# Kernel tuning notes

Measured on AMD Instinct MI355X. Metric: run time of the kernel, lower is better.

The kernel has to match this reference:

```python
import jax, jax.numpy as jnp
import numpy as np

N, T, C_IN, H, C_OUT = 50000, 8, 32, 128, 32
E = 800000


def setup_inputs() -> dict:
    key = jax.random.key(0)
    ks = jax.random.split(key, 16)
    s = 0.05
    return {
        "x": jax.random.normal(ks[0], (N, T, C_IN), dtype=jnp.float32),
        "edge_index": jax.random.randint(ks[1], (2, E), 0, N, dtype=jnp.int64),
        # SAGEConv: lin_l applied to mean-aggregated neighbors (with bias), lin_r to root (no bias)
        "Wl": jax.random.normal(ks[2], (H, C_IN), dtype=jnp.float32) * s,
        "bl": jnp.zeros((H,), dtype=jnp.float32),
        "Wr": jax.random.normal(ks[3], (H, C_IN), dtype=jnp.float32) * s,
        # GRU (torch layout: gates stacked [r; z; n])
        "W_ih": jax.random.normal(ks[4], (3 * H, H), dtype=jnp.float32) * s,
        "b_ih": jnp.zeros((3 * H,), dtype=jnp.float32),
        "W_hh": jax.random.normal(ks[5], (3 * H, H), dtype=jnp.float32) * s,
        "b_hh": jnp.zeros((3 * H,), dtype=jnp.float32),
        # heads
        "W_rec": jax.random.normal(ks[6], (C_OUT, H), dtype=jnp.float32) * s,
        "b_rec": jnp.zeros((C_OUT,), dtype=jnp.float32),
        "W_c1": jax.random.normal(ks[7], (H // 2, H), dtype=jnp.float32) * s,
        "b_c1": jnp.zeros((H // 2,), dtype=jnp.float32),
        "W_c2": jax.random.normal(ks[8], (1, H // 2), dtype=jnp.float32) * s,
        "b_c2": jnp.zeros((1,), dtype=jnp.float32),
    }


def _st_graph_sage(x, edge_index, Wl, bl, Wr, W_ih, b_ih, W_hh, b_hh,
                   W_rec, b_rec, W_c1, b_c1, W_c2, b_c2):
    n_nodes = x.shape[0]
    src, dst = edge_index[0], edge_index[1]
    # in-degree for mean aggregation (avoid div-by-zero for isolated nodes)
    deg = jax.ops.segment_sum(jnp.ones_like(dst, dtype=x.dtype), dst,
                              num_segments=n_nodes)
    deg = jnp.maximum(deg, 1.0)[:, None]
    hdim = W_hh.shape[1]

    def step(h, x_t):
        # SAGEConv (mean aggr): lin_l(mean_j x_j) + lin_r(x_i)
        agg = jax.ops.segment_sum(x_t[src], dst, num_segments=n_nodes) / deg
        sp = jax.nn.relu(agg @ Wl.T + bl + x_t @ Wr.T)
        # single-step GRU (torch equations)
        gx = sp @ W_ih.T + b_ih
        gh = h @ W_hh.T + b_hh
        gx_r, gx_z, gx_n = jnp.split(gx, 3, axis=-1)
        gh_r, gh_z, gh_n = jnp.split(gh, 3, axis=-1)
        r = jax.nn.sigmoid(gx_r + gh_r)
        z = jax.nn.sigmoid(gx_z + gh_z)
        n = jnp.tanh(gx_n + r * gh_n)
        h_new = (1.0 - z) * n + z * h
        return h_new, h_new

    h0 = jnp.zeros((n_nodes, hdim), dtype=x.dtype)
    _, hs = jax.lax.scan(step, h0, jnp.transpose(x, (1, 0, 2)))  # hs: [T, N, H]

    recon = hs @ W_rec.T + b_rec                                  # [T, N, C_OUT]
    cls = jax.nn.sigmoid(jax.nn.relu(hs @ W_c1.T + b_c1) @ W_c2.T + b_c2)  # [T, N, 1]
    reconstruction_output = jnp.transpose(recon, (1, 0, 2))       # [N, T, C_OUT]
    classification_output = jnp.transpose(cls[..., 0], (1, 0))    # [N, T]
    return reconstruction_output, classification_output


def reference(x, edge_index, Wl, bl, Wr, W_ih, b_ih, W_hh, b_hh,
              W_rec, b_rec, W_c1, b_c1, W_c2, b_c2):
    return _st_graph_sage(x, edge_index, Wl, bl, Wr, W_ih, b_ih, W_hh, b_hh,
                          W_rec, b_rec, W_c1, b_c1, W_c2, b_c2)
```

## Files before the change

kernel.cpp:

```cpp
#include <hip/hip_runtime.h>
#include <hip/hip_bf16.h>

#define N_NODES 50000
#define T_STEPS 8
#define CIN     32
#define HDIM    128
#define E_EDGES 800000
#define NBLK    196

typedef __attribute__((ext_vector_type(8))) short  short8;
typedef __attribute__((ext_vector_type(4))) float  f32x4;

__device__ __forceinline__ ushort f2b(float f) {
    __hip_bfloat16 b = __float2bfloat16(f);
    return *reinterpret_cast<ushort*>(&b);
}
__device__ __forceinline__ float b2f(ushort u) { return __uint_as_float(((uint)u) << 16); }
__device__ __forceinline__ float sigm(float x)  { return 1.f / (1.f + __expf(-x)); }
__device__ __forceinline__ float tanhx(float x) { float e = __expf(2.f * x); return 1.f - 2.f / (e + 1.f); }
__device__ __forceinline__ int SW(int fl) { return fl ^ (fl >> 3); }

__global__ void k_deg(const int* __restrict__ ei, int* __restrict__ deg) {
    int e = blockIdx.x * 256 + threadIdx.x;
    if (e < E_EDGES) atomicAdd(&deg[ei[E_EDGES + e]], 1);
}

__global__ __launch_bounds__(256)
void k_scan1(const int* __restrict__ deg, int* __restrict__ incl, int* __restrict__ bsum) {
    __shared__ int sA[256], sB[256];
    int tid = threadIdx.x;
    int i = blockIdx.x * 256 + tid;
    sA[tid] = (i < N_NODES) ? deg[i] : 0;
    __syncthreads();
    int* rd = sA; int* wr = sB;
    for (int off = 1; off < 256; off <<= 1) {
        int v = rd[tid];
        if (tid >= off) v += rd[tid - off];
        wr[tid] = v;
        __syncthreads();
        int* tmp = rd; rd = wr; wr = tmp;
    }
    incl[i] = rd[tid];
    if (tid == 255) bsum[blockIdx.x] = rd[255];
}

__global__ void k_scan2(const int* __restrict__ bsum, int* __restrict__ boff,
                        int* __restrict__ row_ptr) {
    __shared__ int sA[256], sB[256];
    int tid = threadIdx.x;
    int v0 = (tid < NBLK) ? bsum[tid] : 0;
    sA[tid] = v0;
    __syncthreads();
    int* rd = sA; int* wr = sB;
    for (int off = 1; off < 256; off <<= 1) {
        int v = rd[tid];
        if (tid >= off) v += rd[tid - off];
        wr[tid] = v;
        __syncthreads();
        int* tmp = rd; rd = wr; wr = tmp;
    }
    if (tid < NBLK) boff[tid] = rd[tid] - v0;
    if (tid == NBLK - 1) row_ptr[N_NODES] = rd[tid];
}

__global__ __launch_bounds__(256)
void k_scan3(const int* __restrict__ deg, const int* __restrict__ incl,
             const int* __restrict__ boff, int* __restrict__ row_ptr,
             int* __restrict__ cursor, float* __restrict__ rdeg) {
    int i = blockIdx.x * 256 + threadIdx.x;
    if (i >= N_NODES) return;
    int d = deg[i];
    int excl = incl[i] - d + boff[blockIdx.x];
    row_ptr[i] = excl;
    cursor[i]  = excl;
    rdeg[i] = 1.0f / (float)max(d, 1);
}

__global__ void k_bucket(const int* __restrict__ ei, int* __restrict__ cursor,
                         int* __restrict__ csr_src) {
    int e = blockIdx.x * 256 + threadIdx.x;
    if (e < E_EDGES) {
        int d = ei[E_EDGES + e];
        int slot = atomicAdd(&cursor[d], 1);
        csr_src[slot] = ei[e];
    }
}

__global__ __launch_bounds__(256)
void k_xbf(const float* __restrict__ x, ushort* __restrict__ xb) {
    size_t i = ((size_t)blockIdx.x * 256 + threadIdx.x) * 4;
    float4 v = *(const float4*)(x + i);
    ushort4 o; o.x = f2b(v.x); o.y = f2b(v.y); o.z = f2b(v.z); o.w = f2b(v.w);
    *(ushort4*)(xb + i) = o;
}

__global__ void k_pack(const float* __restrict__ Wih, const float* __restrict__ Whh,
                       const float* __restrict__ Wl,  const float* __restrict__ Wr,
                       const float* __restrict__ Wrec,const float* __restrict__ Wc1,
                       short* __restrict__ Bf, short* __restrict__ Bsf, short* __restrict__ B2f) {
    int i = blockIdx.x * 256 + threadIdx.x;
    if (i < 65536) {
        int b = i & 7, lane = (i >> 3) & 63, ks = (i >> 9) & 7, ct = i >> 12;
        int col = ct * 16 + (lane & 15);
        int k = ks * 32 + ((lane >> 4) << 3) + b;
        float v = (k < 128) ? Wih[col * 128 + k] : Whh[col * 128 + (k - 128)];
        Bf[i] = (short)f2b(v);
    } else if (i < 81920) {
        int t2 = i - 65536;
        int b = t2 & 7, lane = (t2 >> 3) & 63, ks = (t2 >> 9) & 3, ct = t2 >> 11;
        int col = 256 + ct * 16 + (lane & 15);
        int k = ks * 32 + ((lane >> 4) << 3) + b;
        Bf[i] = (short)f2b(Wih[col * 128 + k]);
    } else if (i < 98304) {
        int t2 = i - 81920;
        int b = t2 & 7, lane = (t2 >> 3) & 63, ks = (t2 >> 9) & 3, ct = t2 >> 11;
        int col = 256 + ct * 16 + (lane & 15);
        int k = ks * 32 + ((lane >> 4) << 3) + b;
        Bf[i] = (short)f2b(Whh[col * 128 + k]);
    } else if (i < 106496) {
        int t2 = i - 98304;
        int b = t2 & 7, lane = (t2 >> 3) & 63, ks = (t2 >> 9) & 1, ct = t2 >> 10;
        int col = ct * 16 + (lane & 15);
        int k = ks * 32 + ((lane >> 4) << 3) + b;
        float v = (k < 32) ? Wl[col * 32 + k] : Wr[col * 32 + (k - 32)];
        Bsf[t2] = (short)f2b(v);
    } else if (i < 118784) {
        int t3 = i - 106496;
        int b = t3 & 7, lane = (t3 >> 3) & 63, ks = (t3 >> 9) & 3, ct = t3 >> 11;
        int col = ct * 16 + (lane & 15);
        int k = ks * 32 + ((lane >> 4) << 3) + b;
        float v = (col < 32) ? Wrec[col * 128 + k] : Wc1[(col - 32) * 128 + k];
        B2f[t3] = (short)f2b(v);
    }
}

__global__ __launch_bounds__(256)
void k_agg_all(const ushort* __restrict__ xb, const int* __restrict__ row_ptr,
               const int* __restrict__ csr_src, const float* __restrict__ rdeg,
               ushort* __restrict__ aggb) {
    int g = blockIdx.x * 256 + threadIdx.x;
    int node = g >> 3, st = (g & 7) * 4;
    if (node >= N_NODES) return;
    int e0 = row_ptr[node], e1 = row_ptr[node + 1];
    float acc[8][4];
#pragma unroll
    for (int t = 0; t < 8; ++t)
#pragma unroll
        for (int c = 0; c < 4; ++c) acc[t][c] = 0.f;
    for (int e = e0; e < e1; ++e) {
        int s = csr_src[e];
        const ushort* b = xb + (size_t)s * (T_STEPS * CIN) + st;
#pragma unroll
        for (int t = 0; t < 8; ++t) {
            ushort4 v = *(const ushort4*)(b + t * CIN);
            acc[t][0] += b2f(v.x); acc[t][1] += b2f(v.y);
            acc[t][2] += b2f(v.z); acc[t][3] += b2f(v.w);
        }
    }
    float r = rdeg[node];
    ushort* o = aggb + (size_t)node * (T_STEPS * CIN) + st;
#pragma unroll
    for (int t = 0; t < 8; ++t) {
        ushort4 v; v.x = f2b(acc[t][0] * r); v.y = f2b(acc[t][1] * r);
        v.z = f2b(acc[t][2] * r); v.w = f2b(acc[t][3] * r);
        *(ushort4*)(o + t * CIN) = v;
    }
}

template<int RH>
__device__ __forceinline__ void gru_half(const short* lds, const short* __restrict__ Bf,
                                         int wv, int lane, float br_, float bz_,
                                         float bihn, float bhhn, float (&hold)[4][4]) {
    f32x4 accR[2], accZ[2], accN1[2], accN2[2];
#pragma unroll
    for (int ri = 0; ri < 2; ++ri) {
        accR[ri]  = (f32x4){0.f, 0.f, 0.f, 0.f};
        accZ[ri]  = (f32x4){0.f, 0.f, 0.f, 0.f};
        accN1[ri] = (f32x4){0.f, 0.f, 0.f, 0.f};
        accN2[ri] = (f32x4){0.f, 0.f, 0.f, 0.f};
    }
#pragma unroll
    for (int ks = 0; ks < 4; ++ks) {
        short8 av[2];
#pragma unroll
        for (int ri = 0; ri < 2; ++ri)
            av[ri] = *(const short8*)&lds[((ks * 4 + RH * 2 + ri) * 64 + SW(lane)) * 8];
        short8 b0 = *(const short8*)(Bf + (((0 * 8 + wv) * 8 + ks) * 64 + lane) * 8);
        short8 b1 = *(const short8*)(Bf + (((1 * 8 + wv) * 8 + ks) * 64 + lane) * 8);
        short8 bn = *(const short8*)(Bf + (65536 + ((wv * 4 + ks) * 64 + lane) * 8));
#pragma unroll
        for (int ri = 0; ri < 2; ++ri) {
            accR[ri]  = __builtin_amdgcn_mfma_f32_16x16x32_bf16(av[ri], b0, accR[ri], 0, 0, 0);
            accZ[ri]  = __builtin_amdgcn_mfma_f32_16x16x32_bf16(av[ri], b1, accZ[ri], 0, 0, 0);
            accN1[ri] = __builtin_amdgcn_mfma_f32_16x16x32_bf16(av[ri], bn, accN1[ri], 0, 0, 0);
        }
    }
#pragma unroll
    for (int ks = 4; ks < 8; ++ks) {
        short8 av[2];
#pragma unroll
        for (int ri = 0; ri < 2; ++ri)
            av[ri] = *(const short8*)&lds[((ks * 4 + RH * 2 + ri) * 64 + SW(lane)) * 8];
        short8 b0 = *(const short8*)(Bf + (((0 * 8 + wv) * 8 + ks) * 64 + lane) * 8);
        short8 b1 = *(const short8*)(Bf + (((1 * 8 + wv) * 8 + ks) * 64 + lane) * 8);
        short8 bn = *(const short8*)(Bf + (81920 + ((wv * 4 + (ks - 4)) * 64 + lane) * 8));
#pragma unroll
        for (int ri = 0; ri < 2; ++ri) {
            accR[ri]  = __builtin_amdgcn_mfma_f32_16x16x32_bf16(av[ri], b0, accR[ri], 0, 0, 0);
            accZ[ri]  = __builtin_amdgcn_mfma_f32_16x16x32_bf16(av[ri], b1, accZ[ri], 0, 0, 0);
            accN2[ri] = __builtin_amdgcn_mfma_f32_16x16x32_bf16(av[ri], bn, accN2[ri], 0, 0, 0);
        }
    }
#pragma unroll
    for (int ri = 0; ri < 2; ++ri)
#pragma unroll
        for (int q = 0; q < 4; ++q) {
            float r = sigm(accR[ri][q] + br_);
            float z = sigm(accZ[ri][q] + bz_);
            float nn = tanhx(accN1[ri][q] + bihn + r * (accN2[ri][q] + bhhn));
            hold[RH * 2 + ri][q] = (1.f - z) * nn + z * hold[RH * 2 + ri][q];
        }
}

__global__ __launch_bounds__(512, 2)
void k_rec(const ushort* __restrict__ aggb, const ushort* __restrict__ xb,
           const short* __restrict__ Bsf, const short* __restrict__ Bf,
           const short* __restrict__ B2f,
           const float* __restrict__ bl,
           const float* __restrict__ b_ih, const float* __restrict__ b_hh,
           const float* __restrict__ b_rec, const float* __restrict__ b_c1,
           const float* __restrict__ W_c2, const float* __restrict__ b_c2,
           float* __restrict__ out_rec, float* __restrict__ out_cls) {
    __shared__ short lds[28672];
    float* c1f = (float*)&lds[20480];
    const int tid = threadIdx.x;
    const int nb  = blockIdx.x * 64;
    const int wv   = __builtin_amdgcn_readfirstlane(tid >> 6);
    const int lane = tid & 63;
    const int li   = lane & 15, lq = lane >> 4;
    const int j    = wv * 16 + li;

    for (int c = tid; c < 1024; c += 512)
        *(short8*)&lds[8192 + c * 8] = (short8){0, 0, 0, 0, 0, 0, 0, 0};

    float hold[4][4];
#pragma unroll
    for (int ri = 0; ri < 4; ++ri)
#pragma unroll
        for (int q = 0; q < 4; ++q) hold[ri][q] = 0.f;

    const float blc  = bl[j];
    const float br_  = b_ih[j]       + b_hh[j];
    const float bz_  = b_ih[128 + j] + b_hh[128 + j];
    const float bihn = b_ih[256 + j], bhhn = b_hh[256 + j];
    float bhead = 0.f;
    if (wv < 2)      bhead = b_rec[j];
    else if (wv < 6) bhead = b_c1[j - 32];

    const int snode = tid >> 3, sk0 = (tid & 7) * 8;
    const int sgn = nb + snode;
    const ushort* sp0 = nullptr;
    if (sgn < N_NODES)
        sp0 = ((sk0 < 32) ? aggb : xb) + (size_t)sgn * (T_STEPS * CIN) + (sk0 & 31);
    const int sdst = 16384 + (((sk0 >> 5) * 4 + (snode >> 4)) * 64
                              + SW(((sk0 & 31) >> 3) * 16 + (snode & 15))) * 8;
    short8 pv = (short8){0, 0, 0, 0, 0, 0, 0, 0};
    if (sp0) pv = *(const short8*)(sp0);

    auto do_heads = [&](int tt) {
        f32x4 accH[4];
#pragma unroll
        for (int ri = 0; ri < 4; ++ri) accH[ri] = (f32x4){0.f, 0.f, 0.f, 0.f};
#pragma unroll
        for (int ksh = 0; ksh < 4; ++ksh) {
            short8 a[4];
#pragma unroll
            for (int ri = 0; ri < 4; ++ri)
                a[ri] = *(short8*)&lds[(((4 + ksh) * 4 + ri) * 64 + SW(lane)) * 8];
            short8 b = *(const short8*)(B2f + ((wv * 4 + ksh) * 64 + lane) * 8);
#pragma unroll
            for (int ri = 0; ri < 4; ++ri)
                accH[ri] = __builtin_amdgcn_mfma_f32_16x16x32_bf16(a[ri], b, accH[ri], 0, 0, 0);
        }
        if (wv < 2) {
#pragma unroll
            for (int ri = 0; ri < 4; ++ri)
#pragma unroll
                for (int q = 0; q < 4; ++q) {
                    int row = ri * 16 + lq * 4 + q, gn = nb + row;
                    if (gn < N_NODES)
                        out_rec[(size_t)gn * (T_STEPS * 32) + tt * 32 + j] = accH[ri][q] + bhead;
                }
        } else {
            int cc = j - 32;
#pragma unroll
            for (int ri = 0; ri < 4; ++ri)
#pragma unroll
                for (int q = 0; q < 4; ++q) {
                    int row = ri * 16 + lq * 4 + q;
                    c1f[row * 64 + (cc ^ (row & 31))] = fmaxf(accH[ri][q] + bhead, 0.f);
                }
        }
    };
    auto do_cls = [&](int tt) {
        int node = tid >> 3, st = tid & 7, gn2 = nb + node;
        float s = 0.f;
#pragma unroll
        for (int c = 0; c < 8; ++c) {
            int q = st * 8 + c;
            s = fmaf(W_c2[q], c1f[node * 64 + (q ^ (node & 31))], s);
        }
        s += __shfl_xor(s, 1);
        s += __shfl_xor(s, 2);
        s += __shfl_xor(s, 4);
        if (st == 0 && gn2 < N_NODES)
            out_cls[(size_t)gn2 * T_STEPS + tt] = sigm(s + b_c2[0]);
    };

    for (int t = 0; t < T_STEPS; ++t) {
        *(short8*)&lds[sdst] = pv;
        __syncthreads();
        if (sp0 && t + 1 < T_STEPS) pv = *(const short8*)(sp0 + (t + 1) * CIN);

        {
            f32x4 accS[4];
#pragma unroll
            for (int ri = 0; ri < 4; ++ri) accS[ri] = (f32x4){0.f, 0.f, 0.f, 0.f};
#pragma unroll
            for (int ks = 0; ks < 2; ++ks) {
                short8 a[4];
#pragma unroll
                for (int ri = 0; ri < 4; ++ri)
                    a[ri] = *(short8*)&lds[16384 + ((ks * 4 + ri) * 64 + SW(lane)) * 8];
                short8 b = *(const short8*)(Bsf + ((wv * 2 + ks) * 64 + lane) * 8);
#pragma unroll
                for (int ri = 0; ri < 4; ++ri)
                    accS[ri] = __builtin_amdgcn_mfma_f32_16x16x32_bf16(a[ri], b, accS[ri], 0, 0, 0);
            }
            if (t > 0 && wv < 6) do_heads(t - 1);
            int ks_t = j >> 5, lh = (j & 31) >> 3, jj = j & 7;
#pragma unroll
            for (int ri = 0; ri < 4; ++ri)
#pragma unroll
                for (int q = 0; q < 4; ++q) {
                    float v = fmaxf(accS[ri][q] + blc, 0.f);
                    lds[((ks_t * 4 + ri) * 64 + SW(lh * 16 + lq * 4 + q)) * 8 + jj] = (short)f2b(v);
                }
        }
        __syncthreads();

        gru_half<0>(lds, Bf, wv, lane, br_, bz_, bihn, bhhn, hold);
        __builtin_amdgcn_sched_barrier(0);
        gru_half<1>(lds, Bf, wv, lane, br_, bz_, bihn, bhhn, hold);

        if (t > 0) do_cls(t - 1);
        __syncthreads();

        {
            int ks_h = 4 + (j >> 5), lh_h = (j & 31) >> 3, jj_h = j & 7;
#pragma unroll
            for (int ri = 0; ri < 4; ++ri)
#pragma unroll
                for (int q = 0; q < 4; ++q)
                    lds[((ks_h * 4 + ri) * 64 + SW(lh_h * 16 + lq * 4 + q)) * 8 + jj_h]
                        = (short)f2b(hold[ri][q]);
        }
    }

    __syncthreads();
    if (wv < 6) do_heads(T_STEPS - 1);
    __syncthreads();
    do_cls(T_STEPS - 1);
}

extern "C" void kernel_launch(void* const* d_in, const int* in_sizes, int n_in,
                              void* d_out, int out_size, void* d_ws, size_t ws_size,
                              hipStream_t stream) {
    const float* x     = (const float*)d_in[0];
    const int*   ei    = (const int*)  d_in[1];
    const float* Wl    = (const float*)d_in[2];
    const float* bl    = (const float*)d_in[3];
    const float* Wr    = (const float*)d_in[4];
    const float* W_ih  = (const float*)d_in[5];
    const float* b_ih  = (const float*)d_in[6];
    const float* W_hh  = (const float*)d_in[7];
    const float* b_hh  = (const float*)d_in[8];
    const float* W_rec = (const float*)d_in[9];
    const float* b_rec = (const float*)d_in[10];
    const float* W_c1  = (const float*)d_in[11];
    const float* b_c1  = (const float*)d_in[12];
    const float* W_c2  = (const float*)d_in[13];
    const float* b_c2  = (const float*)d_in[14];

    char* wp = (char*)d_ws;
    auto alloc = [&](size_t bytes) -> char* {
        char* p = wp; wp += (bytes + 255) & ~(size_t)255; return p;
    };
    int*    deg     = (int*)   alloc((size_t)N_NODES * 4);
    int*    row_ptr = (int*)   alloc((size_t)(N_NODES + 1) * 4);
    int*    cursor  = (int*)   alloc((size_t)N_NODES * 4);
    int*    csr_src = (int*)   alloc((size_t)E_EDGES * 4);
    float*  rdeg    = (float*) alloc((size_t)N_NODES * 4);
    int*    incl    = (int*)   alloc((size_t)NBLK * 256 * 4);
    int*    bsum    = (int*)   alloc((size_t)256 * 4);
    int*    boff    = (int*)   alloc((size_t)256 * 4);
    short*  Bf      = (short*) alloc((size_t)98304 * 2);
    short*  Bsf     = (short*) alloc((size_t)8192 * 2);
    short*  B2f     = (short*) alloc((size_t)12288 * 2);
    ushort* xb      = (ushort*)alloc((size_t)N_NODES * T_STEPS * CIN * 2);
    ushort* aggb    = (ushort*)alloc((size_t)N_NODES * T_STEPS * CIN * 2);

    float* out_rec = (float*)d_out;
    float* out_cls = out_rec + (size_t)N_NODES * T_STEPS * 32;

    hipMemsetAsync(deg, 0, (size_t)N_NODES * 4, stream);

    k_deg   <<<(E_EDGES + 255) / 256, 256, 0, stream>>>(ei, deg);
    k_scan1 <<<NBLK, 256, 0, stream>>>(deg, incl, bsum);
    k_scan2 <<<1, 256, 0, stream>>>(bsum, boff, row_ptr);
    k_scan3 <<<NBLK, 256, 0, stream>>>(deg, incl, boff, row_ptr, cursor, rdeg);
    k_bucket<<<(E_EDGES + 255) / 256, 256, 0, stream>>>(ei, cursor, csr_src);
    k_xbf   <<<12500, 256, 0, stream>>>(x, xb);
    k_pack  <<<464, 256, 0, stream>>>(W_ih, W_hh, Wl, Wr, W_rec, W_c1, Bf, Bsf, B2f);

    k_agg_all<<<(N_NODES * 8 + 255) / 256, 256, 0, stream>>>(
        xb, row_ptr, csr_src, rdeg, aggb);
    k_rec<<<(N_NODES + 63) / 64, 512, 0, stream>>>(
        aggb, xb, Bsf, Bf, B2f, bl, b_ih, b_hh, b_rec, b_c1, W_c2, b_c2,
        out_rec, out_cls);
}
```

Measured before the change: 447.7 us.

## Process two 64-node tiles per block to amortize weight fragment loads

Each k_rec block now handles 128 nodes as two 64-node tiles, each with its own LDS region and hidden state, held in dynamic shared memory. The GRU step now computes all four row groups at once for each tile instead of two halves, so every B-fragment load from global memory feeds twice as many MFMAs. The aim is to cut repeated weight-fragment global traffic per node. In exchange, register pressure roughly doubles (two hold arrays and 16 accumulators per gate set), LDS use per block doubles, and the grid shrinks, which may lower occupancy or cause spills under launch_bounds(512,2).

```diff
diff --git a/kernel.cpp b/kernel.cpp
--- a/kernel.cpp
+++ b/kernel.cpp
@@ -7,6 +7,7 @@
 #define HDIM    128
 #define E_EDGES 800000
 #define NBLK    196
+#define LDS_T   28672
 
 typedef __attribute__((ext_vector_type(8))) short  short8;
 typedef __attribute__((ext_vector_type(4))) float  f32x4;
@@ -167,61 +168,6 @@
     }
 }
 
-template<int RH>
-__device__ __forceinline__ void gru_half(const short* lds, const short* __restrict__ Bf,
-                                         int wv, int lane, float br_, float bz_,
-                                         float bihn, float bhhn, float (&hold)[4][4]) {
-    f32x4 accR[2], accZ[2], accN1[2], accN2[2];
-#pragma unroll
-    for (int ri = 0; ri < 2; ++ri) {
-        accR[ri]  = (f32x4){0.f, 0.f, 0.f, 0.f};
-        accZ[ri]  = (f32x4){0.f, 0.f, 0.f, 0.f};
-        accN1[ri] = (f32x4){0.f, 0.f, 0.f, 0.f};
-        accN2[ri] = (f32x4){0.f, 0.f, 0.f, 0.f};
-    }
-#pragma unroll
-    for (int ks = 0; ks < 4; ++ks) {
-        short8 av[2];
-#pragma unroll
-        for (int ri = 0; ri < 2; ++ri)
-            av[ri] = *(const short8*)&lds[((ks * 4 + RH * 2 + ri) * 64 + SW(lane)) * 8];
-        short8 b0 = *(const short8*)(Bf + (((0 * 8 + wv) * 8 + ks) * 64 + lane) * 8);
-        short8 b1 = *(const short8*)(Bf + (((1 * 8 + wv) * 8 + ks) * 64 + lane) * 8);
-        short8 bn = *(const short8*)(Bf + (65536 + ((wv * 4 + ks) * 64 + lane) * 8));
-#pragma unroll
-        for (int ri = 0; ri < 2; ++ri) {
-            accR[ri]  = __builtin_amdgcn_mfma_f32_16x16x32_bf16(av[ri], b0, accR[ri], 0, 0, 0);
-            accZ[ri]  = __builtin_amdgcn_mfma_f32_16x16x32_bf16(av[ri], b1, accZ[ri], 0, 0, 0);
-            accN1[ri] = __builtin_amdgcn_mfma_f32_16x16x32_bf16(av[ri], bn, accN1[ri], 0, 0, 0);
-        }
-    }
-#pragma unroll
-    for (int ks = 4; ks < 8; ++ks) {
-        short8 av[2];
-#pragma unroll
-        for (int ri = 0; ri < 2; ++ri)
-            av[ri] = *(const short8*)&lds[((ks * 4 + RH * 2 + ri) * 64 + SW(lane)) * 8];
-        short8 b0 = *(const short8*)(Bf + (((0 * 8 + wv) * 8 + ks) * 64 + lane) * 8);
-        short8 b1 = *(const short8*)(Bf + (((1 * 8 + wv) * 8 + ks) * 64 + lane) * 8);
-        short8 bn = *(const short8*)(Bf + (81920 + ((wv * 4 + (ks - 4)) * 64 + lane) * 8));
-#pragma unroll
-        for (int ri = 0; ri < 2; ++ri) {
-            accR[ri]  = __builtin_amdgcn_mfma_f32_16x16x32_bf16(av[ri], b0, accR[ri], 0, 0, 0);
-            accZ[ri]  = __builtin_amdgcn_mfma_f32_16x16x32_bf16(av[ri], b1, accZ[ri], 0, 0, 0);
-            accN2[ri] = __builtin_amdgcn_mfma_f32_16x16x32_bf16(av[ri], bn, accN2[ri], 0, 0, 0);
-        }
-    }
-#pragma unroll
-    for (int ri = 0; ri < 2; ++ri)
-#pragma unroll
-        for (int q = 0; q < 4; ++q) {
-            float r = sigm(accR[ri][q] + br_);
-            float z = sigm(accZ[ri][q] + bz_);
-            float nn = tanhx(accN1[ri][q] + bihn + r * (accN2[ri][q] + bhhn));
-            hold[RH * 2 + ri][q] = (1.f - z) * nn + z * hold[RH * 2 + ri][q];
-        }
-}
-
 __global__ __launch_bounds__(512, 2)
 void k_rec(const ushort* __restrict__ aggb, const ushort* __restrict__ xb,
            const short* __restrict__ Bsf, const short* __restrict__ Bf,
@@ -231,23 +177,28 @@
            const float* __restrict__ b_rec, const float* __restrict__ b_c1,
            const float* __restrict__ W_c2, const float* __restrict__ b_c2,
            float* __restrict__ out_rec, float* __restrict__ out_cls) {
-    __shared__ short lds[28672];
-    float* c1f = (float*)&lds[20480];
+    extern __shared__ short lds_dyn[];
+    short* const L0 = lds_dyn;
+    short* const L1 = lds_dyn + LDS_T;
+    float* const c1f0 = (float*)&L0[20480];
+    float* const c1f1 = (float*)&L1[20480];
     const int tid = threadIdx.x;
-    const int nb  = blockIdx.x * 64;
+    const int nb  = blockIdx.x * 128;
     const int wv   = __builtin_amdgcn_readfirstlane(tid >> 6);
     const int lane = tid & 63;
     const int li   = lane & 15, lq = lane >> 4;
     const int j    = wv * 16 + li;
 
-    for (int c = tid; c < 1024; c += 512)
-        *(short8*)&lds[8192 + c * 8] = (short8){0, 0, 0, 0, 0, 0, 0, 0};
-
-    float hold[4][4];
+    for (int c = tid; c < 1024; c += 512) {
+        *(short8*)&L0[8192 + c * 8] = (short8){0, 0, 0, 0, 0, 0, 0, 0};
+        *(short8*)&L1[8192 + c * 8] = (short8){0, 0, 0, 0, 0, 0, 0, 0};
+    }
+
+    float hold0[4][4], hold1[4][4];
 #pragma unroll
     for (int ri = 0; ri < 4; ++ri)
 #pragma unroll
-        for (int q = 0; q < 4; ++q) hold[ri][q] = 0.f;
+        for (int q = 0; q < 4; ++q) { hold0[ri][q] = 0.f; hold1[ri][q] = 0.f; }
 
     const float blc  = bl[j];
     const float br_  = b_ih[j]       + b_hh[j];
@@ -258,16 +209,158 @@
     else if (wv < 6) bhead = b_c1[j - 32];
 
     const int snode = tid >> 3, sk0 = (tid & 7) * 8;
-    const int sgn = nb + snode;
+    const int sgn0 = nb + snode, sgn1 = nb + 64 + snode;
     const ushort* sp0 = nullptr;
-    if (sgn < N_NODES)
-        sp0 = ((sk0 < 32) ? aggb : xb) + (size_t)sgn * (T_STEPS * CIN) + (sk0 & 31);
+    const ushort* sp1 = nullptr;
+    if (sgn0 < N_NODES)
+        sp0 = ((sk0 < 32) ? aggb : xb) + (size_t)sgn0 * (T_STEPS * CIN) + (sk0 & 31);
+    if (sgn1 < N_NODES)
+        sp1 = ((sk0 < 32) ? aggb : xb) + (size_t)sgn1 * (T_STEPS * CIN) + (sk0 & 31);
     const int sdst = 16384 + (((sk0 >> 5) * 4 + (snode >> 4)) * 64
                               + SW(((sk0 & 31) >> 3) * 16 + (snode & 15))) * 8;
-    short8 pv = (short8){0, 0, 0, 0, 0, 0, 0, 0};
-    if (sp0) pv = *(const short8*)(sp0);
-
-    auto do_heads = [&](int tt) {
+    short8 pv0 = (short8){0, 0, 0, 0, 0, 0, 0, 0};
+    short8 pv1 = (short8){0, 0, 0, 0, 0, 0, 0, 0};
+    if (sp0) pv0 = *(const short8*)(sp0);
+    if (sp1) pv1 = *(const short8*)(sp1);
+
+    auto p1_tile = [&](short* L, float* c1fT, int t, int nbT) {
+        f32x4 accS[4];
+#pragma unroll
+        for (int ri = 0; ri < 4; ++ri) accS[ri] = (f32x4){0.f, 0.f, 0.f, 0.f};
+#pragma unroll
+        for (int ks = 0; ks < 2; ++ks) {
+            short8 a[4];
+#pragma unroll
+            for (int ri = 0; ri < 4; ++ri)
+                a[ri] = *(short8*)&L[16384 + ((ks * 4 + ri) * 64 + SW(lane)) * 8];
+            short8 b = *(const short8*)(Bsf + ((wv * 2 + ks) * 64 + lane) * 8);
+#pragma unroll
+            for (int ri = 0; ri < 4; ++ri)
+                accS[ri] = __builtin_amdgcn_mfma_f32_16x16x32_bf16(a[ri], b, accS[ri], 0, 0, 0);
+        }
+        if (t > 0 && wv < 6) {
+            f32x4 accH[4];
+#pragma unroll
+            for (int ri = 0; ri < 4; ++ri) accH[ri] = (f32x4){0.f, 0.f, 0.f, 0.f};
+#pragma unroll
+            for (int ksh = 0; ksh < 4; ++ksh) {
+                short8 a[4];
+#pragma unroll
+                for (int ri = 0; ri < 4; ++ri)
+                    a[ri] = *(short8*)&L[(((4 + ksh) * 4 + ri) * 64 + SW(lane)) * 8];
+                short8 b = *(const short8*)(B2f + ((wv * 4 + ksh) * 64 + lane) * 8);
+#pragma unroll
+                for (int ri = 0; ri < 4; ++ri)
+                    accH[ri] = __builtin_amdgcn_mfma_f32_16x16x32_bf16(a[ri], b, accH[ri], 0, 0, 0);
+            }
+            if (wv < 2) {
+#pragma unroll
+                for (int ri = 0; ri < 4; ++ri)
+#pragma unroll
+                    for (int q = 0; q < 4; ++q) {
+                        int row = ri * 16 + lq * 4 + q, gn = nbT + row;
+                        if (gn < N_NODES)
+                            out_rec[(size_t)gn * (T_STEPS * 32) + (t - 1) * 32 + j] = accH[ri][q] + bhead;
+                    }
+            } else {
+                int cc = j - 32;
+#pragma unroll
+                for (int ri = 0; ri < 4; ++ri)
+#pragma unroll
+                    for (int q = 0; q < 4; ++q) {
+                        int row = ri * 16 + lq * 4 + q;
+                        c1fT[row * 64 + (cc ^ (row & 31))] = fmaxf(accH[ri][q] + bhead, 0.f);
+                    }
+            }
+        }
+        int ks_t = j >> 5, lh = (j & 31) >> 3, jj = j & 7;
+#pragma unroll
+        for (int ri = 0; ri < 4; ++ri)
+#pragma unroll
+            for (int q = 0; q < 4; ++q) {
+                float v = fmaxf(accS[ri][q] + blc, 0.f);
+                L[((ks_t * 4 + ri) * 64 + SW(lh * 16 + lq * 4 + q)) * 8 + jj] = (short)f2b(v);
+            }
+    };
+
+    auto gru_tile = [&](short* L, float (&hold)[4][4]) {
+        f32x4 accR[4], accZ[4], accN1[4], accN2[4];
+#pragma unroll
+        for (int ri = 0; ri < 4; ++ri) {
+            accR[ri]  = (f32x4){0.f, 0.f, 0.f, 0.f};
+            accZ[ri]  = (f32x4){0.f, 0.f, 0.f, 0.f};
+            accN1[ri] = (f32x4){0.f, 0.f, 0.f, 0.f};
+            accN2[ri] = (f32x4){0.f, 0.f, 0.f, 0.f};
+        }
+#pragma unroll
+        for (int ks = 0; ks < 4; ++ks) {
+            short8 av[4];
+#pragma unroll
+            for (int ri = 0; ri < 4; ++ri)
+                av[ri] = *(const short8*)&L[((ks * 4 + ri) * 64 + SW(lane)) * 8];
+            short8 b0 = *(const short8*)(Bf + (((0 * 8 + wv) * 8 + ks) * 64 + lane) * 8);
+            short8 b1 = *(const short8*)(Bf + (((1 * 8 + wv) * 8 + ks) * 64 + lane) * 8);
+            short8 bn = *(const short8*)(Bf + (65536 + ((wv * 4 + ks) * 64 + lane) * 8));
+#pragma unroll
+            for (int ri = 0; ri < 4; ++ri) {
+                accR[ri]  = __builtin_amdgcn_mfma_f32_16x16x32_bf16(av[ri], b0, accR[ri], 0, 0, 0);
+                accZ[ri]  = __builtin_amdgcn_mfma_f32_16x16x32_bf16(av[ri], b1, accZ[ri], 0, 0, 0);
+                accN1[ri] = __builtin_amdgcn_mfma_f32_16x16x32_bf16(av[ri], bn, accN1[ri], 0, 0, 0);
+            }
+        }
+#pragma unroll
+        for (int ks = 4; ks < 8; ++ks) {
+            short8 av[4];
+#pragma unroll
+            for (int ri = 0; ri < 4; ++ri)
+                av[ri] = *(const short8*)&L[((ks * 4 + ri) * 64 + SW(lane)) * 8];
+            short8 b0 = *(const short8*)(Bf + (((0 * 8 + wv) * 8 + ks) * 64 + lane) * 8);
+            short8 b1 = *(const short8*)(Bf + (((1 * 8 + wv) * 8 + ks) * 64 + lane) * 8);
+            short8 bn = *(const short8*)(Bf + (81920 + ((wv * 4 + (ks - 4)) * 64 + lane) * 8));
+#pragma unroll
+            for (int ri = 0; ri < 4; ++ri) {
+                accR[ri]  = __builtin_amdgcn_mfma_f32_16x16x32_bf16(av[ri], b0, accR[ri], 0, 0, 0);
+                accZ[ri]  = __builtin_amdgcn_mfma_f32_16x16x32_bf16(av[ri], b1, accZ[ri], 0, 0, 0);
+                accN2[ri] = __builtin_amdgcn_mfma_f32_16x16x32_bf16(av[ri], bn, accN2[ri], 0, 0, 0);
+            }
+        }
+#pragma unroll
+        for (int ri = 0; ri < 4; ++ri)
+#pragma unroll
+            for (int q = 0; q < 4; ++q) {
+                float r = sigm(accR[ri][q] + br_);
+                float z = sigm(accZ[ri][q] + bz_);
+                float nn = tanhx(accN1[ri][q] + bihn + r * (accN2[ri][q] + bhhn));
+                hold[ri][q] = (1.f - z) * nn + z * hold[ri][q];
+            }
+    };
+
+    auto cls_tile = [&](const float* c1fT, int tt, int nbT) {
+        int node = tid >> 3, st = tid & 7, gn2 = nbT + node;
+        float s = 0.f;
+#pragma unroll
+        for (int c = 0; c < 8; ++c) {
+            int q = st * 8 + c;
+            s = fmaf(W_c2[q], c1fT[node * 64 + (q ^ (node & 31))], s);
+        }
+        s += __shfl_xor(s, 1);
+        s += __shfl_xor(s, 2);
+        s += __shfl_xor(s, 4);
+        if (st == 0 && gn2 < N_NODES)
+            out_cls[(size_t)gn2 * T_STEPS + tt] = sigm(s + b_c2[0]);
+    };
+
+    auto hwrite_tile = [&](short* L, const float (&hold)[4][4]) {
+        int ks_h = 4 + (j >> 5), lh_h = (j & 31) >> 3, jj_h = j & 7;
+#pragma unroll
+        for (int ri = 0; ri < 4; ++ri)
+#pragma unroll
+            for (int q = 0; q < 4; ++q)
+                L[((ks_h * 4 + ri) * 64 + SW(lh_h * 16 + lq * 4 + q)) * 8 + jj_h]
+                    = (short)f2b(hold[ri][q]);
+    };
+
+    auto heads_only = [&](short* L, float* c1fT, int tt, int nbT) {
         f32x4 accH[4];
 #pragma unroll
         for (int ri = 0; ri < 4; ++ri) accH[ri] = (f32x4){0.f, 0.f, 0.f, 0.f};
@@ -276,7 +369,7 @@
             short8 a[4];
 #pragma unroll
             for (int ri = 0; ri < 4; ++ri)
-                a[ri] = *(short8*)&lds[(((4 + ksh) * 4 + ri) * 64 + SW(lane)) * 8];
+                a[ri] = *(short8*)&L[(((4 + ksh) * 4 + ri) * 64 + SW(lane)) * 8];
             short8 b = *(const short8*)(B2f + ((wv * 4 + ksh) * 64 + lane) * 8);
 #pragma unroll
             for (int ri = 0; ri < 4; ++ri)
@@ -287,7 +380,7 @@
             for (int ri = 0; ri < 4; ++ri)
 #pragma unroll
                 for (int q = 0; q < 4; ++q) {
-                    int row = ri * 16 + lq * 4 + q, gn = nb + row;
+                    int row = ri * 16 + lq * 4 + q, gn = nbT + row;
                     if (gn < N_NODES)
                         out_rec[(size_t)gn * (T_STEPS * 32) + tt * 32 + j] = accH[ri][q] + bhead;
                 }
@@ -298,79 +391,38 @@
 #pragma unroll
                 for (int q = 0; q < 4; ++q) {
                     int row = ri * 16 + lq * 4 + q;
-                    c1f[row * 64 + (cc ^ (row & 31))] = fmaxf(accH[ri][q] + bhead, 0.f);
+                    c1fT[row * 64 + (cc ^ (row & 31))] = fmaxf(accH[ri][q] + bhead, 0.f);
                 }
         }
     };
-    auto do_cls = [&](int tt) {
-        int node = tid >> 3, st = tid & 7, gn2 = nb + node;
-        float s = 0.f;
-#pragma unroll
-        for (int c = 0; c < 8; ++c) {
-            int q = st * 8 + c;
-            s = fmaf(W_c2[q], c1f[node * 64 + (q ^ (node & 31))], s);
-        }
-        s += __shfl_xor(s, 1);
-        s += __shfl_xor(s, 2);
-        s += __shfl_xor(s, 4);
-        if (st == 0 && gn2 < N_NODES)
-            out_cls[(size_t)gn2 * T_STEPS + tt] = sigm(s + b_c2[0]);
-    };
 
     for (int t = 0; t < T_STEPS; ++t) {
-        *(short8*)&lds[sdst] = pv;
+        *(short8*)&L0[sdst] = pv0;
+        *(short8*)&L1[sdst] = pv1;
         __syncthreads();
-        if (sp0 && t + 1 < T_STEPS) pv = *(const short8*)(sp0 + (t + 1) * CIN);
-
-        {
-            f32x4 accS[4];
-#pragma unroll
-            for (int ri = 0; ri < 4; ++ri) accS[ri] = (f32x4){0.f, 0.f, 0.f, 0.f};
-#pragma unroll
-            for (int ks = 0; ks < 2; ++ks) {
-                short8 a[4];
-#pragma unroll
-                for (int ri = 0; ri < 4; ++ri)
-                    a[ri] = *(short8*)&lds[16384 + ((ks * 4 + ri) * 64 + SW(lane)) * 8];
-                short8 b = *(const short8*)(Bsf + ((wv * 2 + ks) * 64 + lane) * 8);
-#pragma unroll
-                for (int ri = 0; ri < 4; ++ri)
-                    accS[ri] = __builtin_amdgcn_mfma_f32_16x16x32_bf16(a[ri], b, accS[ri], 0, 0, 0);
-            }
-            if (t > 0 && wv < 6) do_heads(t - 1);
-            int ks_t = j >> 5, lh = (j & 31) >> 3, jj = j & 7;
-#pragma unroll
-            for (int ri = 0; ri < 4; ++ri)
-#pragma unroll
-                for (int q = 0; q < 4; ++q) {
-                    float v = fmaxf(accS[ri][q] + blc, 0.f);
-                    lds[((ks_t * 4 + ri) * 64 + SW(lh * 16 + lq * 4 + q)) * 8 + jj] = (short)f2b(v);
-                }
-        }
+        if (t + 1 < T_STEPS) {
+            if (sp0) pv0 = *(const short8*)(sp0 + (t + 1) * CIN);
+            if (sp1) pv1 = *(const short8*)(sp1 + (t + 1) * CIN);
+        }
+
+        p1_tile(L0, c1f0, t, nb);
+        p1_tile(L1, c1f1, t, nb + 64);
         __syncthreads();
 
-        gru_half<0>(lds, Bf, wv, lane, br_, bz_, bihn, bhhn, hold);
-        __builtin_amdgcn_sched_barrier(0);
-        gru_half<1>(lds, Bf, wv, lane, br_, bz_, bihn, bhhn, hold);
-
-        if (t > 0) do_cls(t - 1);
+        gru_tile(L0, hold0);
+        gru_tile(L1, hold1);
+        if (t > 0) { cls_tile(c1f0, t - 1, nb); cls_tile(c1f1, t - 1, nb + 64); }
         __syncthreads();
 
-        {
-            int ks_h = 4 + (j >> 5), lh_h = (j & 31) >> 3, jj_h = j & 7;
-#pragma unroll
-            for (int ri = 0; ri < 4; ++ri)
-#pragma unroll
-                for (int q = 0; q < 4; ++q)
-                    lds[((ks_h * 4 + ri) * 64 + SW(lh_h * 16 + lq * 4 + q)) * 8 + jj_h]
-                        = (short)f2b(hold[ri][q]);
-        }
+        hwrite_tile(L0, hold0);
+        hwrite_tile(L1, hold1);
     }
 
     __syncthreads();
-    if (wv < 6) do_heads(T_STEPS - 1);
+    if (wv < 6) { heads_only(L0, c1f0, T_STEPS - 1, nb); heads_only(L1, c1f1, T_STEPS - 1, nb + 64); }
     __syncthreads();
-    do_cls(T_STEPS - 1);
+    cls_tile(c1f0, T_STEPS - 1, nb);
+    cls_tile(c1f1, T_STEPS - 1, nb + 64);
 }
 
 extern "C" void kernel_launch(void* const* d_in, const int* in_sizes, int n_in,
@@ -425,7 +477,11 @@
 
     k_agg_all<<<(N_NODES * 8 + 255) / 256, 256, 0, stream>>>(
         xb, row_ptr, csr_src, rdeg, aggb);
-    k_rec<<<(N_NODES + 63) / 64, 512, 0, stream>>>(
+
+    const int kRecLds = 2 * LDS_T * 2;
+    hipFuncSetAttribute((const void*)k_rec,
+                        hipFuncAttributeMaxDynamicSharedMemorySize, kRecLds);
+    k_rec<<<(N_NODES + 127) / 128, 512, kRecLds, stream>>>(
         aggb, xb, Bsf, Bf, B2f, bl, b_ih, b_hh, b_rec, b_c1, W_c2, b_c2,
         out_rec, out_cls);
 }
```

New measurement: 842.6 us. +88.2%, slower.

## Halve k_rec block to 256 threads with each wave owning two column tiles

Applied to the files above, without the earlier changes.

The recurrent kernel now runs 4 waves per block instead of 8. Each wave handles two 16-column tiles of the SAGE, GRU and head matmuls, and keeps two sets of hidden-state registers. The classification intermediate in LDS moves from fp32 to bf16, which shrinks shared memory from 56KB to 48KB, and launch bounds change to allow three blocks per CU. The aim is better occupancy and more independent MFMA work per wave. The cost is higher register pressure per thread, which may spill, and extra rounding of the classifier hidden layer.

```diff
diff --git a/kernel.cpp b/kernel.cpp
--- a/kernel.cpp
+++ b/kernel.cpp
@@ -7,6 +7,9 @@
 #define HDIM    128
 #define E_EDGES 800000
 #define NBLK    196
+
+#define AS_BASE 16384
+#define C1_BASE 20480
 
 typedef __attribute__((ext_vector_type(8))) short  short8;
 typedef __attribute__((ext_vector_type(4))) float  f32x4;
@@ -168,9 +171,11 @@
 }
 
 template<int RH>
-__device__ __forceinline__ void gru_half(const short* lds, const short* __restrict__ Bf,
-                                         int wv, int lane, float br_, float bz_,
-                                         float bihn, float bhhn, float (&hold)[4][4]) {
+__device__ __forceinline__ void gru_sub(const short* lds, const short* __restrict__ Bf,
+                                        int swl, int lane,
+                                        int ctr, int ctz, int ctn,
+                                        float br_, float bz_,
+                                        float bihn, float bhhn, float (&hold)[4][4]) {
     f32x4 accR[2], accZ[2], accN1[2], accN2[2];
 #pragma unroll
     for (int ri = 0; ri < 2; ++ri) {
@@ -184,10 +189,10 @@
         short8 av[2];
 #pragma unroll
         for (int ri = 0; ri < 2; ++ri)
-            av[ri] = *(const short8*)&lds[((ks * 4 + RH * 2 + ri) * 64 + SW(lane)) * 8];
-        short8 b0 = *(const short8*)(Bf + (((0 * 8 + wv) * 8 + ks) * 64 + lane) * 8);
-        short8 b1 = *(const short8*)(Bf + (((1 * 8 + wv) * 8 + ks) * 64 + lane) * 8);
-        short8 bn = *(const short8*)(Bf + (65536 + ((wv * 4 + ks) * 64 + lane) * 8));
+            av[ri] = *(const short8*)&lds[((ks * 4 + RH * 2 + ri) * 64 + swl) * 8];
+        short8 b0 = *(const short8*)(Bf + ((ctr * 8 + ks) * 64 + lane) * 8);
+        short8 b1 = *(const short8*)(Bf + ((ctz * 8 + ks) * 64 + lane) * 8);
+        short8 bn = *(const short8*)(Bf + (65536 + ((ctn * 4 + ks) * 64 + lane) * 8));
 #pragma unroll
         for (int ri = 0; ri < 2; ++ri) {
             accR[ri]  = __builtin_amdgcn_mfma_f32_16x16x32_bf16(av[ri], b0, accR[ri], 0, 0, 0);
@@ -196,14 +201,14 @@
         }
     }
 #pragma unroll
-    for (int ks = 4; ks < 8; ++ks) {
+    for (int kk = 0; kk < 4; ++kk) {
         short8 av[2];
 #pragma unroll
         for (int ri = 0; ri < 2; ++ri)
-            av[ri] = *(const short8*)&lds[((ks * 4 + RH * 2 + ri) * 64 + SW(lane)) * 8];
-        short8 b0 = *(const short8*)(Bf + (((0 * 8 + wv) * 8 + ks) * 64 + lane) * 8);
-        short8 b1 = *(const short8*)(Bf + (((1 * 8 + wv) * 8 + ks) * 64 + lane) * 8);
-        short8 bn = *(const short8*)(Bf + (81920 + ((wv * 4 + (ks - 4)) * 64 + lane) * 8));
+            av[ri] = *(const short8*)&lds[(((4 + kk) * 4 + RH * 2 + ri) * 64 + swl) * 8];
+        short8 b0 = *(const short8*)(Bf + ((ctr * 8 + 4 + kk) * 64 + lane) * 8);
+        short8 b1 = *(const short8*)(Bf + ((ctz * 8 + 4 + kk) * 64 + lane) * 8);
+        short8 bn = *(const short8*)(Bf + (81920 + ((ctn * 4 + kk) * 64 + lane) * 8));
 #pragma unroll
         for (int ri = 0; ri < 2; ++ri) {
             accR[ri]  = __builtin_amdgcn_mfma_f32_16x16x32_bf16(av[ri], b0, accR[ri], 0, 0, 0);
@@ -222,7 +227,7 @@
         }
 }
 
-__global__ __launch_bounds__(512, 2)
+__global__ __launch_bounds__(256, 3)
 void k_rec(const ushort* __restrict__ aggb, const ushort* __restrict__ xb,
            const short* __restrict__ Bsf, const short* __restrict__ Bf,
            const short* __restrict__ B2f,
@@ -231,43 +236,81 @@
            const float* __restrict__ b_rec, const float* __restrict__ b_c1,
            const float* __restrict__ W_c2, const float* __restrict__ b_c2,
            float* __restrict__ out_rec, float* __restrict__ out_cls) {
-    __shared__ short lds[28672];
-    float* c1f = (float*)&lds[20480];
+    __shared__ short lds[24576];
+    short* const c1b = &lds[C1_BASE];
     const int tid = threadIdx.x;
     const int nb  = blockIdx.x * 64;
     const int wv   = __builtin_amdgcn_readfirstlane(tid >> 6);
     const int lane = tid & 63;
     const int li   = lane & 15, lq = lane >> 4;
-    const int j    = wv * 16 + li;
-
-    for (int c = tid; c < 1024; c += 512)
+    const int swl  = SW(lane);
+
+    for (int c = tid; c < 1024; c += 256)
         *(short8*)&lds[8192 + c * 8] = (short8){0, 0, 0, 0, 0, 0, 0, 0};
 
-    float hold[4][4];
+    float hold0[4][4], hold1[4][4];
 #pragma unroll
     for (int ri = 0; ri < 4; ++ri)
 #pragma unroll
-        for (int q = 0; q < 4; ++q) hold[ri][q] = 0.f;
-
-    const float blc  = bl[j];
-    const float br_  = b_ih[j]       + b_hh[j];
-    const float bz_  = b_ih[128 + j] + b_hh[128 + j];
-    const float bihn = b_ih[256 + j], bhhn = b_hh[256 + j];
-    float bhead = 0.f;
-    if (wv < 2)      bhead = b_rec[j];
-    else if (wv < 6) bhead = b_c1[j - 32];
-
-    const int snode = tid >> 3, sk0 = (tid & 7) * 8;
-    const int sgn = nb + snode;
-    const ushort* sp0 = nullptr;
-    if (sgn < N_NODES)
-        sp0 = ((sk0 < 32) ? aggb : xb) + (size_t)sgn * (T_STEPS * CIN) + (sk0 & 31);
-    const int sdst = 16384 + (((sk0 >> 5) * 4 + (snode >> 4)) * 64
-                              + SW(((sk0 & 31) >> 3) * 16 + (snode & 15))) * 8;
-    short8 pv = (short8){0, 0, 0, 0, 0, 0, 0, 0};
-    if (sp0) pv = *(const short8*)(sp0);
-
-    auto do_heads = [&](int tt) {
+        for (int q = 0; q < 4; ++q) { hold0[ri][q] = 0.f; hold1[ri][q] = 0.f; }
+
+    const int j0 = wv * 16 + li, j1 = 64 + j0;
+    const int ctr0 = wv, ctz0 = 8 + wv, ctn0 = wv;
+    const int ctr1 = 4 + wv, ctz1 = 12 + wv, ctn1 = 4 + wv;
+    const float blc0 = bl[j0], blc1 = bl[j1];
+    const float br0 = b_ih[j0] + b_hh[j0],          bz0 = b_ih[128 + j0] + b_hh[128 + j0];
+    const float bihn0 = b_ih[256 + j0],             bhhn0 = b_hh[256 + j0];
+    const float br1 = b_ih[j1] + b_hh[j1],          bz1 = b_ih[128 + j1] + b_hh[128 + j1];
+    const float bihn1 = b_ih[256 + j1],             bhhn1 = b_hh[256 + j1];
+    float bh0 = 0.f, bh1 = 0.f;
+    if (wv < 3) {
+        int c0 = wv * 16 + li;
+        bh0 = (wv < 2) ? b_rec[c0] : b_c1[c0 - 32];
+        bh1 = b_c1[(wv + 3) * 16 + li - 32];
+    }
+
+    const int u1i = tid + 256;
+    const int sn0 = tid >> 3, sk0 = (tid & 7) * 8;
+    const int sn1 = u1i >> 3, sk1 = (u1i & 7) * 8;
+    const ushort* spA = nullptr; const ushort* spB = nullptr;
+    if (nb + sn0 < N_NODES)
+        spA = ((sk0 < 32) ? aggb : xb) + (size_t)(nb + sn0) * (T_STEPS * CIN) + (sk0 & 31);
+    if (nb + sn1 < N_NODES)
+        spB = ((sk1 < 32) ? aggb : xb) + (size_t)(nb + sn1) * (T_STEPS * CIN) + (sk1 & 31);
+    const int sdA = AS_BASE + (((sk0 >> 5) * 4 + (sn0 >> 4)) * 64
+                               + SW(((sk0 & 31) >> 3) * 16 + (sn0 & 15))) * 8;
+    const int sdB = AS_BASE + (((sk1 >> 5) * 4 + (sn1 >> 4)) * 64
+                               + SW(((sk1 & 31) >> 3) * 16 + (sn1 & 15))) * 8;
+    short8 pvA = (short8){0,0,0,0,0,0,0,0}, pvB = (short8){0,0,0,0,0,0,0,0};
+    if (spA) pvA = *(const short8*)(spA);
+    if (spB) pvB = *(const short8*)(spB);
+
+    auto do_sage_ct = [&](int ct, float blc) {
+        f32x4 accS[4];
+#pragma unroll
+        for (int ri = 0; ri < 4; ++ri) accS[ri] = (f32x4){0.f, 0.f, 0.f, 0.f};
+#pragma unroll
+        for (int ks = 0; ks < 2; ++ks) {
+            short8 a[4];
+#pragma unroll
+            for (int ri = 0; ri < 4; ++ri)
+                a[ri] = *(short8*)&lds[AS_BASE + ((ks * 4 + ri) * 64 + swl) * 8];
+            short8 b = *(const short8*)(Bsf + ((ct * 2 + ks) * 64 + lane) * 8);
+#pragma unroll
+            for (int ri = 0; ri < 4; ++ri)
+                accS[ri] = __builtin_amdgcn_mfma_f32_16x16x32_bf16(a[ri], b, accS[ri], 0, 0, 0);
+        }
+        int j = ct * 16 + li;
+        int ks_t = j >> 5, lh = (j & 31) >> 3, jj = j & 7;
+#pragma unroll
+        for (int ri = 0; ri < 4; ++ri)
+#pragma unroll
+            for (int q = 0; q < 4; ++q) {
+                float v = fmaxf(accS[ri][q] + blc, 0.f);
+                lds[((ks_t * 4 + ri) * 64 + SW(lh * 16 + lq * 4 + q)) * 8 + jj] = (short)f2b(v);
+            }
+    };
+    auto do_heads_ct = [&](int ct, float bh, int tt) {
         f32x4 accH[4];
 #pragma unroll
         for (int ri = 0; ri < 4; ++ri) accH[ri] = (f32x4){0.f, 0.f, 0.f, 0.f};
@@ -276,99 +319,89 @@
             short8 a[4];
 #pragma unroll
             for (int ri = 0; ri < 4; ++ri)
-                a[ri] = *(short8*)&lds[(((4 + ksh) * 4 + ri) * 64 + SW(lane)) * 8];
-            short8 b = *(const short8*)(B2f + ((wv * 4 + ksh) * 64 + lane) * 8);
+                a[ri] = *(short8*)&lds[(((4 + ksh) * 4 + ri) * 64 + swl) * 8];
+            short8 b = *(const short8*)(B2f + ((ct * 4 + ksh) * 64 + lane) * 8);
 #pragma unroll
             for (int ri = 0; ri < 4; ++ri)
                 accH[ri] = __builtin_amdgcn_mfma_f32_16x16x32_bf16(a[ri], b, accH[ri], 0, 0, 0);
         }
-        if (wv < 2) {
+        int col = ct * 16 + li;
+        if (col < 32) {
 #pragma unroll
             for (int ri = 0; ri < 4; ++ri)
 #pragma unroll
                 for (int q = 0; q < 4; ++q) {
                     int row = ri * 16 + lq * 4 + q, gn = nb + row;
                     if (gn < N_NODES)
-                        out_rec[(size_t)gn * (T_STEPS * 32) + tt * 32 + j] = accH[ri][q] + bhead;
+                        out_rec[(size_t)gn * (T_STEPS * 32) + tt * 32 + col] = accH[ri][q] + bh;
                 }
         } else {
-            int cc = j - 32;
+            int cc = col - 32;
 #pragma unroll
             for (int ri = 0; ri < 4; ++ri)
 #pragma unroll
                 for (int q = 0; q < 4; ++q) {
                     int row = ri * 16 + lq * 4 + q;
-                    c1f[row * 64 + (cc ^ (row & 31))] = fmaxf(accH[ri][q] + bhead, 0.f);
+                    c1b[row * 64 + (cc ^ (row & 31))] = (short)f2b(fmaxf(accH[ri][q] + bh, 0.f));
                 }
         }
     };
     auto do_cls = [&](int tt) {
-        int node = tid >> 3, st = tid & 7, gn2 = nb + node;
+        int node = tid >> 2, st = tid & 3, gn2 = nb + node;
         float s = 0.f;
 #pragma unroll
-        for (int c = 0; c < 8; ++c) {
-            int q = st * 8 + c;
-            s = fmaf(W_c2[q], c1f[node * 64 + (q ^ (node & 31))], s);
+        for (int c = 0; c < 16; ++c) {
+            int q = st * 16 + c;
+            s = fmaf(W_c2[q], b2f((ushort)c1b[node * 64 + (q ^ (node & 31))]), s);
         }
         s += __shfl_xor(s, 1);
         s += __shfl_xor(s, 2);
-        s += __shfl_xor(s, 4);
         if (st == 0 && gn2 < N_NODES)
             out_cls[(size_t)gn2 * T_STEPS + tt] = sigm(s + b_c2[0]);
     };
+    auto hwrite_g = [&](int j, const float (&hold)[4][4]) {
+        int ks_h = 4 + (j >> 5), lh_h = (j & 31) >> 3, jj_h = j & 7;
+#pragma unroll
+        for (int ri = 0; ri < 4; ++ri)
+#pragma unroll
+            for (int q = 0; q < 4; ++q)
+                lds[((ks_h * 4 + ri) * 64 + SW(lh_h * 16 + lq * 4 + q)) * 8 + jj_h]
+                    = (short)f2b(hold[ri][q]);
+    };
 
     for (int t = 0; t < T_STEPS; ++t) {
-        *(short8*)&lds[sdst] = pv;
+        *(short8*)&lds[sdA] = pvA;
+        *(short8*)&lds[sdB] = pvB;
         __syncthreads();
-        if (sp0 && t + 1 < T_STEPS) pv = *(const short8*)(sp0 + (t + 1) * CIN);
-
-        {
-            f32x4 accS[4];
-#pragma unroll
-            for (int ri = 0; ri < 4; ++ri) accS[ri] = (f32x4){0.f, 0.f, 0.f, 0.f};
-#pragma unroll
-            for (int ks = 0; ks < 2; ++ks) {
-                short8 a[4];
-#pragma unroll
-                for (int ri = 0; ri < 4; ++ri)
-                    a[ri] = *(short8*)&lds[16384 + ((ks * 4 + ri) * 64 + SW(lane)) * 8];
-                short8 b = *(const short8*)(Bsf + ((wv * 2 + ks) * 64 + lane) * 8);
-#pragma unroll
-                for (int ri = 0; ri < 4; ++ri)
-                    accS[ri] = __builtin_amdgcn_mfma_f32_16x16x32_bf16(a[ri], b, accS[ri], 0, 0, 0);
-            }
-            if (t > 0 && wv < 6) do_heads(t - 1);
-            int ks_t = j >> 5, lh = (j & 31) >> 3, jj = j & 7;
-#pragma unroll
-            for (int ri = 0; ri < 4; ++ri)
-#pragma unroll
-                for (int q = 0; q < 4; ++q) {
-                    float v = fmaxf(accS[ri][q] + blc, 0.f);
-                    lds[((ks_t * 4 + ri) * 64 + SW(lh * 16 + lq * 4 + q)) * 8 + jj] = (short)f2b(v);
-                }
-        }
+        if (t + 1 < T_STEPS) {
+            if (spA) pvA = *(const short8*)(spA + (t + 1) * CIN);
+            if (spB) pvB = *(const short8*)(spB + (t + 1) * CIN);
+        }
+
+        if (t > 0 && wv < 3) {
+            do_heads_ct(wv, bh0, t - 1);
+            do_heads_ct(wv + 3, bh1, t - 1);
+        }
+        do_sage_ct(wv, blc0);
+        do_sage_ct(wv + 4, blc1);
         __syncthreads();
 
-        gru_half<0>(lds, Bf, wv, lane, br_, bz_, bihn, bhhn, hold);
-        __builtin_amdgcn_sched_barrier(0);
-        gru_half<1>(lds, Bf, wv, lane, br_, bz_, bihn, bhhn, hold);
-
+        gru_sub<0>(lds, Bf, swl, lane, ctr0, ctz0, ctn0, br0, bz0, bihn0, bhhn0, hold0);
+        gru_sub<1>(lds, Bf, swl, lane, ctr0, ctz0, ctn0, br0, bz0, bihn0, bhhn0, hold0);
+        gru_sub<0>(lds, Bf, swl, lane, ctr1, ctz1, ctn1, br1, bz1, bihn1, bhhn1, hold1);
+        gru_sub<1>(lds, Bf, swl, lane, ctr1, ctz1, ctn1, br1, bz1, bihn1, bhhn1, hold1);
         if (t > 0) do_cls(t - 1);
         __syncthreads();
 
-        {
-            int ks_h = 4 + (j >> 5), lh_h = (j & 31) >> 3, jj_h = j & 7;
-#pragma unroll
-            for (int ri = 0; ri < 4; ++ri)
-#pragma unroll
-                for (int q = 0; q < 4; ++q)
-                    lds[((ks_h * 4 + ri) * 64 + SW(lh_h * 16 + lq * 4 + q)) * 8 + jj_h]
-                        = (short)f2b(hold[ri][q]);
-        }
+        hwrite_g(j0, hold0);
+        hwrite_g(j1, hold1);
     }
 
     __syncthreads();
-    if (wv < 6) do_heads(T_STEPS - 1);
+    if (wv < 3) {
+        do_heads_ct(wv, bh0, T_STEPS - 1);
+        do_heads_ct(wv + 3, bh1, T_STEPS - 1);
+    }
     __syncthreads();
     do_cls(T_STEPS - 1);
 }
@@ -425,7 +458,8 @@
 
     k_agg_all<<<(N_NODES * 8 + 255) / 256, 256, 0, stream>>>(
         xb, row_ptr, csr_src, rdeg, aggb);
-    k_rec<<<(N_NODES + 63) / 64, 512, 0, stream>>>(
+
+    k_rec<<<(N_NODES + 63) / 64, 256, 0, stream>>>(
         aggb, xb, Bsf, Bf, B2f, bl, b_ih, b_hh, b_rec, b_c1, W_c2, b_c2,
         out_rec, out_cls);
 }
```

Result: slower. 1.225 ms (+173.7%).
